# Performance work log

Measured on AMD Instinct MI355X. Metric: run time of the kernel, lower is better.

Reference implementation:

```python
import jax, jax.numpy as jnp
import numpy as np

N_NODES = 50000
N_EDGES = 600000
D_IN = 128
D_OUT = 128
N_BASES = 4
N_RATINGS = 5


def setup_inputs() -> dict:
    key = jax.random.key(0)
    k1, k2, k3, k4, k5, k6 = jax.random.split(key, 6)
    x = jax.random.normal(k1, (N_NODES, D_IN), dtype=jnp.float32)
    edge_index = jax.random.randint(k2, (2, N_EDGES), 0, N_NODES, dtype=jnp.int64)
    edge_type = jax.random.randint(k3, (N_EDGES,), 0, N_RATINGS, dtype=jnp.int64)
    # basis matrices B_k: (out, in); a_r stacked over ratings: (R, K); W_0: (out, in)
    B = jax.random.normal(k4, (N_BASES, D_OUT, D_IN), dtype=jnp.float32) * 0.05
    A = jax.random.normal(k5, (N_RATINGS, N_BASES), dtype=jnp.float32) * 0.05
    W0 = jax.random.normal(k6, (D_OUT, D_IN), dtype=jnp.float32) * 0.05
    return {"x": x, "edge_index": edge_index, "edge_type": edge_type, "B": B, "A": A, "W0": W0}


def reference(x, edge_index, edge_type, B, A, W0):
    # self-loop term: (W0 @ x^T)^T == x @ W0^T
    n_nodes = x.shape[0]
    src, tgt = edge_index[0], edge_index[1]
    out = x @ W0.T  # [N, out]
    # per-relation basis-composed weights W_r = sum_k a_r[k] * B_k  -> [R, out, in]
    W = jnp.einsum('rk,kod->rod', A, B)
    n_ratings = A.shape[0]
    for r in range(n_ratings):  # small fixed relation set
        h = x @ W[r].T                     # [N, out] transform once per node
        msg = jnp.where((edge_type == r)[:, None], h[src], jnp.float32(0))  # [E, out]
        out = out + jax.ops.segment_sum(msg, tgt, num_segments=n_nodes)
    return out
```

## Files before the change

### kernel.cpp

```cpp
#include <hip/hip_runtime.h>

#define N_NODES 50000
#define N_EDGES 600000
#define D 128
#define KTOT 768
#define NB_SCAN 196

typedef __attribute__((ext_vector_type(8))) short short8;
typedef __attribute__((ext_vector_type(4))) float float4v;

static __device__ __forceinline__ float bf2f(unsigned int u16) {
    union { unsigned int i; float f; } v; v.i = u16 << 16; return v.f;
}
static __device__ __forceinline__ unsigned short f2bf(float f) {
    union { float f; unsigned int i; } v; v.f = f;
    unsigned int u = v.i;
    return (unsigned short)((u + 0x7FFFu + ((u >> 16) & 1u)) >> 16);
}
static __device__ __forceinline__ float h2f(unsigned int h) {
    unsigned int s = (h >> 15) & 1u, e = (h >> 10) & 0x1fu, m = h & 0x3ffu;
    unsigned int bits = (e == 0) ? (s << 31)
                                 : ((s << 31) | ((e + 112u) << 23) | (m << 13));
    union { unsigned int i; float f; } v; v.i = bits; return v.f;
}

__global__ __launch_bounds__(256) void setup(int* __restrict__ flags,
                                             int* __restrict__ cnt,
                                             unsigned int* __restrict__ scanst) {
    int i = blockIdx.x * 256 + threadIdx.x;
    if (i < N_NODES) cnt[i] = 0;
    if (i < 8) flags[i] = 0;
    if (i < 200) scanst[i] = 0;
}

__global__ __launch_bounds__(256) void detect_all(const int* __restrict__ ei,
                                                  const int* __restrict__ et,
                                                  const unsigned int* __restrict__ x,
                                                  const unsigned int* __restrict__ B,
                                                  const unsigned int* __restrict__ A,
                                                  const unsigned int* __restrict__ W0,
                                                  int* __restrict__ flags) {
    __shared__ int sflag;
    if (threadIdx.x == 0) sflag = 0;
    __syncthreads();
    int b = blockIdx.x, acc = 0, fidx;
    if (b < 192) {
        fidx = 0;
        for (int i = b * 256 + threadIdx.x; i < N_EDGES; i += 192 * 256)
            acc |= ei[2 * i + 1];
    } else if (b < 240) {
        fidx = 1;
        for (int i = (b - 192) * 256 + threadIdx.x; i < N_EDGES / 2; i += 48 * 256)
            acc |= et[2 * i + 1];
    } else if (b < 288) {
        fidx = 2;
        for (int i = (b - 240) * 256 + threadIdx.x; i < 600000; i += 48 * 256) {
            unsigned int e = (x[i] >> 7) & 0xffu;
            acc |= (e > 0xA0u || e < 0x50u) ? 1 : 0;
        }
    } else if (b < 300) {
        fidx = 3;
        for (int i = (b - 288) * 256 + threadIdx.x; i < 32768; i += 12 * 256) {
            unsigned int e = (B[i] >> 7) & 0xffu;
            acc |= (e > 0xA0u || e < 0x50u) ? 1 : 0;
        }
    } else if (b == 300) {
        fidx = 4;
        for (int i = threadIdx.x; i < 10; i += 256) {
            unsigned int e = (A[i] >> 7) & 0xffu;
            acc |= (e > 0xA0u || e < 0x50u) ? 1 : 0;
        }
    } else if (b < 307) {
        fidx = 5;
        for (int i = (b - 301) * 256 + threadIdx.x; i < 8192; i += 6 * 256) {
            unsigned int e = (W0[i] >> 7) & 0xffu;
            acc |= (e > 0xA0u || e < 0x50u) ? 1 : 0;
        }
    } else {
        fidx = 6;
        for (int i = (b - 307) * 256 + threadIdx.x; i < 300000; i += 48 * 256) {
            unsigned int el = (x[i] >> 7) & 0xffu, eh = (x[i] >> 23) & 0xffu;
            acc |= (el < 0x58u || eh < 0x58u) ? 1 : 0;
        }
    }
    if (acc) sflag = 1;
    __syncthreads();
    if (threadIdx.x == 0 && sflag) atomicOr(flags + fidx, 1);
}

static __device__ __forceinline__ float loadw(const void* p, int idx, int f32) {
    return f32 ? ((const float*)p)[idx] : bf2f(((const unsigned short*)p)[idx]);
}

__global__ __launch_bounds__(256) void norm_hist_conv(const int* __restrict__ ei,
                                                      const int* __restrict__ et,
                                                      int* __restrict__ idx32,
                                                      int* __restrict__ et32,
                                                      int* __restrict__ cnt,
                                                      const void* __restrict__ A,
                                                      const void* __restrict__ B,
                                                      const void* __restrict__ W0,
                                                      unsigned short* __restrict__ wcatB,
                                                      const void* __restrict__ xraw,
                                                      unsigned short* __restrict__ Xcat,
                                                      const int* __restrict__ flags) {
    int b = blockIdx.x;
    if (b < 4688) {
        int i = b * 256 + threadIdx.x;
        if (i < 2 * N_EDGES) {
            int v = flags[0] ? ei[i] : ei[2 * i];
            idx32[i] = v;
            if (i >= N_EDGES && (unsigned)v < (unsigned)N_NODES)
                atomicAdd(&cnt[v], 1);
        }
    } else if (b < 7032) {
        int i = (b - 4688) * 256 + threadIdx.x;
        if (i < N_EDGES) et32[i] = flags[1] ? et[i] : et[2 * i];
    } else if (b < 7416) {
        int idx = (b - 7032) * 256 + threadIdx.x;
        int fB = flags[3], fA = flags[4], fW = flags[5];
        int o = idx / KTOT, k = idx % KTOT;
        float v;
        if (k < D) {
            v = loadw(W0, o * D + k, fW);
        } else {
            int r = (k - D) >> 7, d = (k - D) & 127;
            v = 0.f;
#pragma unroll
            for (int j = 0; j < 4; ++j)
                v += loadw(A, r * 4 + j, fA) * loadw(B, (j * D + o) * D + d, fB);
        }
        wcatB[idx] = f2bf(v);
    } else {
        int idx = (b - 7416) * 256 + threadIdx.x;
        int n = idx >> 5, cg = idx & 31;
        int f32 = flags[2], f16 = flags[6];
        unsigned short o0, o1, o2, o3;
        if (f32) {
            float4 v = *((const float4*)xraw + idx);
            o0 = f2bf(v.x); o1 = f2bf(v.y); o2 = f2bf(v.z); o3 = f2bf(v.w);
        } else {
            uint2 v = *((const uint2*)xraw + idx);
            if (f16) {
                o0 = f2bf(h2f(v.x & 0xffffu)); o1 = f2bf(h2f(v.x >> 16));
                o2 = f2bf(h2f(v.y & 0xffffu)); o3 = f2bf(h2f(v.y >> 16));
            } else {
                o0 = v.x & 0xffffu; o1 = v.x >> 16; o2 = v.y & 0xffffu; o3 = v.y >> 16;
            }
        }
        unsigned long long pack = (unsigned long long)o0 | ((unsigned long long)o1 << 16) |
                                  ((unsigned long long)o2 << 32) | ((unsigned long long)o3 << 48);
        *(unsigned long long*)(Xcat + (size_t)n * KTOT + cg * 4) = pack;
    }
}

__global__ __launch_bounds__(256) void prep_wt6_direct(const void* __restrict__ A,
                                                       const void* __restrict__ B,
                                                       const void* __restrict__ W0,
                                                       float* __restrict__ wcatT6F,
                                                       const int* __restrict__ flags) {
    int idx = blockIdx.x * 256 + threadIdx.x;
    int fB = flags[3], fA = flags[4], fW = flags[5];
    int slot = idx >> 14, d = (idx >> 7) & 127, o = idx & 127;
    float v;
    if (slot == 0) {
        v = loadw(W0, o * D + d, fW);
    } else {
        int r = slot - 1;
        v = 0.f;
#pragma unroll
        for (int j = 0; j < 4; ++j)
            v += loadw(A, r * 4 + j, fA) * loadw(B, (j * D + o) * D + d, fB);
    }
    wcatT6F[idx] = v;
}

#define SC_AGG (1u << 30)
#define SC_PRE (1u << 31)
__global__ __launch_bounds__(256) void scan_fused(const int* __restrict__ cnt,
                                                  int* __restrict__ offsets,
                                                  int* __restrict__ cursor,
                                                  unsigned int* __restrict__ scanst) {
    __shared__ int sh[256];
    __shared__ int sbid, sprefix;
    unsigned int* status = scanst;
    unsigned int* ticket = scanst + 196;
    int t = threadIdx.x;
    if (t == 0) sbid = (int)atomicAdd(ticket, 1u);
    __syncthreads();
    int bid = sbid;
    int idx = bid * 256 + t;
    int v = (idx < N_NODES) ? cnt[idx] : 0;
    sh[t] = v;
    __syncthreads();
    for (int off = 1; off < 256; off <<= 1) {
        int a = (t >= off) ? sh[t - off] : 0;
        __syncthreads();
        sh[t] += a;
        __syncthreads();
    }
    if (t == 0) {
        int total = sh[255];
        atomicExch(&status[bid], (unsigned int)total | SC_AGG);
        int prefix = 0;
        for (int j = bid - 1; j >= 0; --j) {
            unsigned int s;
            do { s = atomicAdd(&status[j], 0u); } while ((s & (SC_AGG | SC_PRE)) == 0u);
            prefix += (int)(s & 0x3FFFFFFFu);
            if (s & SC_PRE) break;
        }
        atomicExch(&status[bid], (unsigned int)(prefix + total) | SC_PRE);
        sprefix = prefix;
    }
    __syncthreads();
    int excl = sh[t] - v + sprefix;
    if (idx < N_NODES) {
        offsets[idx] = excl;
        cursor[idx] = excl;
        if (idx == N_NODES - 1) offsets[N_NODES] = excl + v;
    }
}

__global__ __launch_bounds__(256) void place(const int* __restrict__ src,
                                             const int* __restrict__ tgt,
                                             const int* __restrict__ et,
                                             int* __restrict__ cursor,
                                             int* __restrict__ entries) {
    int e = blockIdx.x * 256 + threadIdx.x;
    if (e >= N_EDGES) return;
    int s = src[e], g = tgt[e], r = et[e];
    if ((unsigned)s >= (unsigned)N_NODES || (unsigned)g >= (unsigned)N_NODES || (unsigned)r >= 5u) return;
    int pos = atomicAdd(&cursor[g], 1);
    entries[pos] = s * 8 + r;
}

#define AGG_ACC2(ent, xw)                                            \
    {                                                                \
        int r_ = (ent) & 7;                                          \
        float flo_ = __uint_as_float((xw) << 16);                    \
        float fhi_ = __uint_as_float((xw) & 0xffff0000u);            \
        if (r_ == 0)      { a0 += flo_; a1 += fhi_; }                \
        else if (r_ == 1) { b0 += flo_; b1 += fhi_; }                \
        else if (r_ == 2) { c0 += flo_; c1 += fhi_; }                \
        else if (r_ == 3) { d0 += flo_; d1 += fhi_; }                \
        else              { e0 += flo_; e1 += fhi_; }                \
    }

static __device__ __forceinline__ unsigned int agg_row_load(
        const unsigned int* __restrict__ Xcat32, int ent, int lane) {
    unsigned int row = (unsigned int)(ent >> 3);
    if (row >= (unsigned)N_NODES) row = 0u;
    return Xcat32[(size_t)row * 384 + lane];
}

__global__ __launch_bounds__(256) void aggregate(const int* __restrict__ offsets,
                                                 const int* __restrict__ entries,
                                                 unsigned int* __restrict__ Xcat32) {
    int tid = threadIdx.x;
    int wid = tid >> 6, lane = tid & 63;
    int n = __builtin_amdgcn_readfirstlane(blockIdx.x * 4 + wid);
    int beg = __builtin_amdgcn_readfirstlane(offsets[n]);
    int end = __builtin_amdgcn_readfirstlane(offsets[n + 1]);
    float a0 = 0, a1 = 0, b0 = 0, b1 = 0, c0 = 0, c1 = 0, d0 = 0, d1 = 0, e0 = 0, e1 = 0;

    for (int base = beg; base < end; base += 64) {
        int cnt = end - base;
        if (cnt > 64) cnt = 64;
        int eload = entries[base + lane];
        int j = 0;
        for (; j + 3 < cnt; j += 4) {
            int en0 = __builtin_amdgcn_readlane(eload, j);
            int en1 = __builtin_amdgcn_readlane(eload, j + 1);
            int en2 = __builtin_amdgcn_readlane(eload, j + 2);
            int en3 = __builtin_amdgcn_readlane(eload, j + 3);
            unsigned int x0 = agg_row_load(Xcat32, en0, lane);
            unsigned int x1 = agg_row_load(Xcat32, en1, lane);
            unsigned int x2 = agg_row_load(Xcat32, en2, lane);
            unsigned int x3 = agg_row_load(Xcat32, en3, lane);
            AGG_ACC2(en0, x0);
            AGG_ACC2(en1, x1);
            AGG_ACC2(en2, x2);
            AGG_ACC2(en3, x3);
        }
        for (; j < cnt; ++j) {
            int en = __builtin_amdgcn_readlane(eload, j);
            unsigned int xw = agg_row_load(Xcat32, en, lane);
            AGG_ACC2(en, xw);
        }
    }

    size_t o = (size_t)n * 384 + 64 + lane;
    Xcat32[o]       = (unsigned int)f2bf(a0) | ((unsigned int)f2bf(a1) << 16);
    Xcat32[o + 64]  = (unsigned int)f2bf(b0) | ((unsigned int)f2bf(b1) << 16);
    Xcat32[o + 128] = (unsigned int)f2bf(c0) | ((unsigned int)f2bf(c1) << 16);
    Xcat32[o + 192] = (unsigned int)f2bf(d0) | ((unsigned int)f2bf(d1) << 16);
    Xcat32[o + 256] = (unsigned int)f2bf(e0) | ((unsigned int)f2bf(e1) << 16);
}

__global__ __launch_bounds__(256) void gemm_mfma(const unsigned short* __restrict__ Xcat,
                                                 const unsigned short* __restrict__ wcatB,
                                                 float* __restrict__ outF) {
    __shared__ unsigned short xs[128 * 72];
    __shared__ unsigned short wsd[128 * 72];
    int tid = threadIdx.x;
    int m0 = blockIdx.x * 128;
    int wid = tid >> 6, lane = tid & 63;
    int wm = (wid & 1) * 64, wn = (wid >> 1) * 64;
    int lm = lane & 15, kg = lane >> 4;
    int srow = tid >> 3, scol = (tid & 7) * 8;

    float4v accf[4][4];
#pragma unroll
    for (int i = 0; i < 4; ++i)
#pragma unroll
        for (int j = 0; j < 4; ++j) accf[i][j] = (float4v){0.f, 0.f, 0.f, 0.f};

    short8 xr[4], wr[4];
    const short8 z8 = {0, 0, 0, 0, 0, 0, 0, 0};
#pragma unroll
    for (int i = 0; i < 4; ++i) {
        int row = srow + i * 32;
        int gm = m0 + row;
        xr[i] = (gm < N_NODES) ? *(const short8*)(Xcat + (size_t)gm * KTOT + scol) : z8;
        wr[i] = *(const short8*)(wcatB + (size_t)row * KTOT + scol);
    }

    for (int kc = 0; kc < 12; ++kc) {
        if (kc) __syncthreads();
#pragma unroll
        for (int i = 0; i < 4; ++i) {
            int row = srow + i * 32;
            *(short8*)(&xs[row * 72 + scol]) = xr[i];
            *(short8*)(&wsd[row * 72 + scol]) = wr[i];
        }
        __syncthreads();
        if (kc + 1 < 12) {
            int kb = (kc + 1) * 64 + scol;
#pragma unroll
            for (int i = 0; i < 4; ++i) {
                int row = srow + i * 32;
                int gm = m0 + row;
                xr[i] = (gm < N_NODES) ? *(const short8*)(Xcat + (size_t)gm * KTOT + kb) : z8;
                wr[i] = *(const short8*)(wcatB + (size_t)row * KTOT + kb);
            }
        }
#pragma unroll
        for (int kb = 0; kb < 2; ++kb) {
            int k = kb * 32 + kg * 8;
            short8 a[4], b[4];
#pragma unroll
            for (int i = 0; i < 4; ++i)
                a[i] = *(const short8*)(&xs[(wm + i * 16 + lm) * 72 + k]);
#pragma unroll
            for (int j = 0; j < 4; ++j)
                b[j] = *(const short8*)(&wsd[(wn + j * 16 + lm) * 72 + k]);
#pragma unroll
            for (int i = 0; i < 4; ++i)
#pragma unroll
                for (int j = 0; j < 4; ++j)
                    accf[i][j] = __builtin_amdgcn_mfma_f32_16x16x32_bf16(a[i], b[j], accf[i][j], 0, 0, 0);
        }
    }

#pragma unroll
    for (int i = 0; i < 4; ++i) {
        int gmb = m0 + wm + i * 16 + kg * 4;
#pragma unroll
        for (int j = 0; j < 4; ++j) {
            int gn = wn + j * 16 + lm;
#pragma unroll
            for (int r = 0; r < 4; ++r) {
                int gm = gmb + r;
                if (gm < N_NODES) outF[(size_t)gm * D + gn] = accf[i][j][r];
            }
        }
    }
}

static __device__ __forceinline__ float2 readx2(const void* x, int node, int lane,
                                                int f32, int f16) {
    if (f32) return *((const float2*)x + (size_t)node * 64 + lane);
    unsigned int w = *((const unsigned int*)x + (size_t)node * 64 + lane);
    float2 r;
    if (f16) { r.x = h2f(w & 0xffffu); r.y = h2f(w >> 16); }
    else     { r.x = bf2f(w & 0xffffu); r.y = bf2f(w >> 16); }
    return r;
}

__global__ __launch_bounds__(256) void self_raw(const void* __restrict__ x,
                                                const float* __restrict__ wcatT6F,
                                                float* __restrict__ outF,
                                                const int* __restrict__ flags) {
    int t = blockIdx.x * 256 + threadIdx.x;
    int n = t >> 6, lane = t & 63;
    int f32 = flags[2], f16 = flags[6];
    float2 xp = readx2(x, n, lane, f32, f16);
    float m0 = 0.f, m1 = 0.f;
#pragma unroll 8
    for (int dp = 0; dp < 64; ++dp) {
        float xa = __shfl(xp.x, dp);
        float xc = __shfl(xp.y, dp);
        float2 w0 = *(const float2*)(wcatT6F + (size_t)(2 * dp) * D + 2 * lane);
        float2 w1 = *(const float2*)(wcatT6F + (size_t)(2 * dp + 1) * D + 2 * lane);
        m0 += xa * w0.x + xc * w1.x;
        m1 += xa * w0.y + xc * w1.y;
    }
    *((float2*)outF + (size_t)n * 64 + lane) = make_float2(m0, m1);
}

__global__ __launch_bounds__(256) void edge_raw(const int* __restrict__ src,
                                                const int* __restrict__ tgt,
                                                const int* __restrict__ et,
                                                const void* __restrict__ x,
                                                const float* __restrict__ wcatT6F,
                                                float* __restrict__ outF,
                                                const int* __restrict__ flags) {
    int t = blockIdx.x * 256 + threadIdx.x;
    int e = t >> 6, lane = t & 63;
    if (e >= N_EDGES) return;
    int f32 = flags[2], f16 = flags[6];
    int s = src[e], g = tgt[e], r = et[e];
    if ((unsigned)s >= (unsigned)N_NODES || (unsigned)g >= (unsigned)N_NODES || (unsigned)r >= 5u) return;
    float2 xp = readx2(x, s, lane, f32, f16);
    const float* wt = wcatT6F + (size_t)(1 + r) * D * D;
    float m0 = 0.f, m1 = 0.f;
#pragma unroll 8
    for (int dp = 0; dp < 64; ++dp) {
        float xa = __shfl(xp.x, dp);
        float xc = __shfl(xp.y, dp);
        float2 w0 = *(const float2*)(wt + (size_t)(2 * dp) * D + 2 * lane);
        float2 w1 = *(const float2*)(wt + (size_t)(2 * dp + 1) * D + 2 * lane);
        m0 += xa * w0.x + xc * w1.x;
        m1 += xa * w0.y + xc * w1.y;
    }
    float* ap = outF + (size_t)g * D + lane * 2;
    atomicAdd(ap + 0, m0);
    atomicAdd(ap + 1, m1);
}

extern "C" void kernel_launch(void* const* d_in, const int* in_sizes, int n_in,
                              void* d_out, int out_size, void* d_ws, size_t ws_size,
                              hipStream_t stream) {
    const void* x  = nullptr; const int* ei = nullptr; const int* et = nullptr;
    const void* B  = nullptr; const void* A = nullptr; const void* W0 = nullptr;
    for (int i = 0; i < n_in; ++i) {
        switch (in_sizes[i]) {
            case 6400000: x  = d_in[i]; break;
            case 1200000: ei = (const int*)d_in[i]; break;
            case 600000:  et = (const int*)d_in[i]; break;
            case 65536:   B  = d_in[i]; break;
            case 20:      A  = d_in[i]; break;
            case 16384:   W0 = d_in[i]; break;
            default: break;
        }
    }
    if (!x || !ei || !et || !B || !A || !W0) {
        x  = d_in[0]; ei = (const int*)d_in[1]; et = (const int*)d_in[2];
        B  = d_in[3]; A  = d_in[4]; W0 = d_in[5];
    }
    float* outF = (float*)d_out;

    char* ws = (char*)d_ws;
    int*   flags   = (int*)(ws + 0);
    float* wcatT6F = (float*)(ws + 256);
    unsigned short* wcatB = (unsigned short*)(ws + 393472);
    int* offsets  = (int*)(ws + 590080);
    int* cursor   = (int*)(ws + 790144);
    int* cnt      = (int*)(ws + 990144);
    unsigned int* scanst = (unsigned int*)(ws + 1190144);
    int* entries  = (int*)(ws + 1191168);
    int* idx32    = (int*)(ws + 3591168);
    int* et32     = (int*)(ws + 8391168);
    unsigned short* Xcat = (unsigned short*)(ws + 10791168);
    const size_t needMain = 10791168ull + 76800000ull;
    const size_t needT3   = 393472ull;

    int* src32 = idx32;
    int* tgt32 = idx32 + N_EDGES;

    setup<<<NB_SCAN, 256, 0, stream>>>(flags, cnt, scanst);
    detect_all<<<355, 256, 0, stream>>>(ei, et, (const unsigned int*)x,
                                        (const unsigned int*)B, (const unsigned int*)A,
                                        (const unsigned int*)W0, flags);

    if (ws_size >= needMain) {
        norm_hist_conv<<<13666, 256, 0, stream>>>(ei, et, idx32, et32, cnt,
                                                  A, B, W0, wcatB, x, Xcat, flags);
        scan_fused<<<NB_SCAN, 256, 0, stream>>>(cnt, offsets, cursor, scanst);
        place<<<2344, 256, 0, stream>>>(src32, tgt32, et32, cursor, entries);
        aggregate<<<12500, 256, 0, stream>>>(offsets, entries, (unsigned int*)Xcat);
        gemm_mfma<<<391, 256, 0, stream>>>(Xcat, wcatB, outF);
    } else if (ws_size >= needT3) {
        prep_wt6_direct<<<384, 256, 0, stream>>>(A, B, W0, wcatT6F, flags);
        self_raw<<<12500, 256, 0, stream>>>(x, wcatT6F, outF, flags);
        edge_raw<<<150000, 256, 0, stream>>>(ei, ei + N_EDGES, et, x, wcatT6F, outF, flags);
    }
}
```

Baseline: 228.5 us.

## Transform nodes first, then gather per-relation transformed rows into output

Reorders the computation from aggregate-then-GEMM to GEMM-then-aggregate. A new MFMA GEMM computes Y = x·[W0;W1..W5]^T per node in bf16 (768 columns). The aggregation then gathers the relation-specific slice of Y for each incoming edge and adds the self term, writing fp32 output directly. This removes the separate x→Xcat conversion and the final 768-K GEMM. The scan and place kernels are merged into one using a grid-wide spin barrier, which depends on all 196 blocks being resident at once. Results are now rounded to bf16 per transformed message before summation, which changes numerics.

```diff
diff --git a/kernel.cpp b/kernel.cpp
--- a/kernel.cpp
+++ b/kernel.cpp
@@ -3,7 +3,6 @@
 #define N_NODES 50000
 #define N_EDGES 600000
 #define D 128
-#define KTOT 768
 #define NB_SCAN 196
 
 typedef __attribute__((ext_vector_type(8))) short short8;
@@ -92,18 +91,16 @@
     return f32 ? ((const float*)p)[idx] : bf2f(((const unsigned short*)p)[idx]);
 }
 
-__global__ __launch_bounds__(256) void norm_hist_conv(const int* __restrict__ ei,
-                                                      const int* __restrict__ et,
-                                                      int* __restrict__ idx32,
-                                                      int* __restrict__ et32,
-                                                      int* __restrict__ cnt,
-                                                      const void* __restrict__ A,
-                                                      const void* __restrict__ B,
-                                                      const void* __restrict__ W0,
-                                                      unsigned short* __restrict__ wcatB,
-                                                      const void* __restrict__ xraw,
-                                                      unsigned short* __restrict__ Xcat,
-                                                      const int* __restrict__ flags) {
+__global__ __launch_bounds__(256) void norm_hist_w(const int* __restrict__ ei,
+                                                   const int* __restrict__ et,
+                                                   int* __restrict__ idx32,
+                                                   int* __restrict__ et32,
+                                                   int* __restrict__ cnt,
+                                                   const void* __restrict__ A,
+                                                   const void* __restrict__ B,
+                                                   const void* __restrict__ W0,
+                                                   unsigned short* __restrict__ wcatW,
+                                                   const int* __restrict__ flags) {
     int b = blockIdx.x;
     if (b < 4688) {
         int i = b * 256 + threadIdx.x;
@@ -116,41 +113,22 @@
     } else if (b < 7032) {
         int i = (b - 4688) * 256 + threadIdx.x;
         if (i < N_EDGES) et32[i] = flags[1] ? et[i] : et[2 * i];
-    } else if (b < 7416) {
+    } else {
         int idx = (b - 7032) * 256 + threadIdx.x;
         int fB = flags[3], fA = flags[4], fW = flags[5];
-        int o = idx / KTOT, k = idx % KTOT;
+        int f = idx >> 7, d = idx & 127;
+        int slot = f >> 7, o = f & 127;
         float v;
-        if (k < D) {
-            v = loadw(W0, o * D + k, fW);
+        if (slot == 0) {
+            v = loadw(W0, o * D + d, fW);
         } else {
-            int r = (k - D) >> 7, d = (k - D) & 127;
+            int r = slot - 1;
             v = 0.f;
 #pragma unroll
             for (int j = 0; j < 4; ++j)
                 v += loadw(A, r * 4 + j, fA) * loadw(B, (j * D + o) * D + d, fB);
         }
-        wcatB[idx] = f2bf(v);
-    } else {
-        int idx = (b - 7416) * 256 + threadIdx.x;
-        int n = idx >> 5, cg = idx & 31;
-        int f32 = flags[2], f16 = flags[6];
-        unsigned short o0, o1, o2, o3;
-        if (f32) {
-            float4 v = *((const float4*)xraw + idx);
-            o0 = f2bf(v.x); o1 = f2bf(v.y); o2 = f2bf(v.z); o3 = f2bf(v.w);
-        } else {
-            uint2 v = *((const uint2*)xraw + idx);
-            if (f16) {
-                o0 = f2bf(h2f(v.x & 0xffffu)); o1 = f2bf(h2f(v.x >> 16));
-                o2 = f2bf(h2f(v.y & 0xffffu)); o3 = f2bf(h2f(v.y >> 16));
-            } else {
-                o0 = v.x & 0xffffu; o1 = v.x >> 16; o2 = v.y & 0xffffu; o3 = v.y >> 16;
-            }
-        }
-        unsigned long long pack = (unsigned long long)o0 | ((unsigned long long)o1 << 16) |
-                                  ((unsigned long long)o2 << 32) | ((unsigned long long)o3 << 48);
-        *(unsigned long long*)(Xcat + (size_t)n * KTOT + cg * 4) = pack;
+        wcatW[idx] = f2bf(v);
     }
 }
 
@@ -175,16 +153,131 @@
     wcatT6F[idx] = v;
 }
 
+__global__ __launch_bounds__(256) void gemm_y(const void* __restrict__ xraw,
+                                              const unsigned short* __restrict__ wcatW,
+                                              unsigned short* __restrict__ Ybf,
+                                              const int* __restrict__ flags) {
+    __shared__ unsigned short xs[64 * 136];
+    __shared__ unsigned short wsd[128 * 136];
+    int tid = threadIdx.x;
+    int m0 = blockIdx.x * 64;
+    int wid = tid >> 6, lane = tid & 63;
+    int wm = (wid & 1) * 32, wn = (wid >> 1) * 64;
+    int lm = lane & 15, kg = lane >> 4;
+    int f32 = flags[2], f16 = flags[6];
+    const short8 z8 = {0, 0, 0, 0, 0, 0, 0, 0};
+
+    {
+        int row = tid >> 2, cseg = (tid & 3) * 32;
+        int gm = m0 + row;
+        short8 av[4];
+        if (gm >= N_NODES) {
+#pragma unroll
+            for (int q = 0; q < 4; ++q) av[q] = z8;
+        } else if (f32) {
+            const float4* xp = (const float4*)xraw + (((size_t)gm * D + cseg) >> 2);
+#pragma unroll
+            for (int q = 0; q < 4; ++q) {
+                float4 u0 = xp[2 * q], u1 = xp[2 * q + 1];
+                union { short8 s; unsigned short h[8]; } pk;
+                pk.h[0] = f2bf(u0.x); pk.h[1] = f2bf(u0.y);
+                pk.h[2] = f2bf(u0.z); pk.h[3] = f2bf(u0.w);
+                pk.h[4] = f2bf(u1.x); pk.h[5] = f2bf(u1.y);
+                pk.h[6] = f2bf(u1.z); pk.h[7] = f2bf(u1.w);
+                av[q] = pk.s;
+            }
+        } else if (f16) {
+            const uint4* xp4 = (const uint4*)xraw + (((size_t)gm * D + cseg) >> 3);
+#pragma unroll
+            for (int q = 0; q < 4; ++q) {
+                uint4 u = xp4[q];
+                unsigned int ww[4] = {u.x, u.y, u.z, u.w};
+                union { short8 s; unsigned short h[8]; } pk;
+#pragma unroll
+                for (int z = 0; z < 4; ++z) {
+                    pk.h[2 * z]     = f2bf(h2f(ww[z] & 0xffffu));
+                    pk.h[2 * z + 1] = f2bf(h2f(ww[z] >> 16));
+                }
+                av[q] = pk.s;
+            }
+        } else {
+            const uint4* xp4 = (const uint4*)xraw + (((size_t)gm * D + cseg) >> 3);
+#pragma unroll
+            for (int q = 0; q < 4; ++q) {
+                union { uint4 v; short8 s; } cv; cv.v = xp4[q];
+                av[q] = cv.s;
+            }
+        }
+#pragma unroll
+        for (int q = 0; q < 4; ++q)
+            *(short8*)(&xs[row * 136 + cseg + q * 8]) = av[q];
+    }
+
+    for (int nt = 0; nt < 6; ++nt) {
+        if (nt) __syncthreads();
+        {
+            int row = tid >> 1, cseg = (tid & 1) * 64;
+            const unsigned short* wp = wcatW + (size_t)(nt * 128 + row) * D + cseg;
+#pragma unroll
+            for (int q = 0; q < 8; ++q)
+                *(short8*)(&wsd[row * 136 + cseg + q * 8]) = *(const short8*)(wp + q * 8);
+        }
+        __syncthreads();
+
+        float4v accf[2][4];
+#pragma unroll
+        for (int i = 0; i < 2; ++i)
+#pragma unroll
+            for (int j = 0; j < 4; ++j) accf[i][j] = (float4v){0.f, 0.f, 0.f, 0.f};
+
+#pragma unroll
+        for (int kb = 0; kb < 4; ++kb) {
+            int k = kb * 32 + kg * 8;
+            short8 a[2], b[4];
+#pragma unroll
+            for (int i = 0; i < 2; ++i)
+                a[i] = *(const short8*)(&xs[(wm + i * 16 + lm) * 136 + k]);
+#pragma unroll
+            for (int j = 0; j < 4; ++j)
+                b[j] = *(const short8*)(&wsd[(wn + j * 16 + lm) * 136 + k]);
+#pragma unroll
+            for (int i = 0; i < 2; ++i)
+#pragma unroll
+                for (int j = 0; j < 4; ++j)
+                    accf[i][j] = __builtin_amdgcn_mfma_f32_16x16x32_bf16(a[i], b[j], accf[i][j], 0, 0, 0);
+        }
+
+#pragma unroll
+        for (int i = 0; i < 2; ++i) {
+            int gmb = m0 + wm + i * 16 + kg * 4;
+#pragma unroll
+            for (int j = 0; j < 4; ++j) {
+                int gn = nt * 128 + wn + j * 16 + lm;
+#pragma unroll
+                for (int r = 0; r < 4; ++r) {
+                    int gm = gmb + r;
+                    if (gm < N_NODES) Ybf[(size_t)gm * 768 + gn] = f2bf(accf[i][j][r]);
+                }
+            }
+        }
+    }
+}
+
 #define SC_AGG (1u << 30)
 #define SC_PRE (1u << 31)
-__global__ __launch_bounds__(256) void scan_fused(const int* __restrict__ cnt,
+__global__ __launch_bounds__(256) void scan_place(const int* __restrict__ cnt,
                                                   int* __restrict__ offsets,
                                                   int* __restrict__ cursor,
-                                                  unsigned int* __restrict__ scanst) {
+                                                  unsigned int* __restrict__ scanst,
+                                                  const int* __restrict__ src,
+                                                  const int* __restrict__ tgt,
+                                                  const int* __restrict__ et,
+                                                  int* __restrict__ entries) {
     __shared__ int sh[256];
     __shared__ int sbid, sprefix;
     unsigned int* status = scanst;
     unsigned int* ticket = scanst + 196;
+    unsigned int* done   = scanst + 197;
     int t = threadIdx.x;
     if (t == 0) sbid = (int)atomicAdd(ticket, 1u);
     __syncthreads();
@@ -216,52 +309,36 @@
     int excl = sh[t] - v + sprefix;
     if (idx < N_NODES) {
         offsets[idx] = excl;
-        cursor[idx] = excl;
+        atomicExch(&cursor[idx], excl);
         if (idx == N_NODES - 1) offsets[N_NODES] = excl + v;
     }
-}
-
-__global__ __launch_bounds__(256) void place(const int* __restrict__ src,
-                                             const int* __restrict__ tgt,
-                                             const int* __restrict__ et,
-                                             int* __restrict__ cursor,
-                                             int* __restrict__ entries) {
-    int e = blockIdx.x * 256 + threadIdx.x;
-    if (e >= N_EDGES) return;
-    int s = src[e], g = tgt[e], r = et[e];
-    if ((unsigned)s >= (unsigned)N_NODES || (unsigned)g >= (unsigned)N_NODES || (unsigned)r >= 5u) return;
-    int pos = atomicAdd(&cursor[g], 1);
-    entries[pos] = s * 8 + r;
-}
-
-#define AGG_ACC2(ent, xw)                                            \
-    {                                                                \
-        int r_ = (ent) & 7;                                          \
-        float flo_ = __uint_as_float((xw) << 16);                    \
-        float fhi_ = __uint_as_float((xw) & 0xffff0000u);            \
-        if (r_ == 0)      { a0 += flo_; a1 += fhi_; }                \
-        else if (r_ == 1) { b0 += flo_; b1 += fhi_; }                \
-        else if (r_ == 2) { c0 += flo_; c1 += fhi_; }                \
-        else if (r_ == 3) { d0 += flo_; d1 += fhi_; }                \
-        else              { e0 += flo_; e1 += fhi_; }                \
-    }
-
-static __device__ __forceinline__ unsigned int agg_row_load(
-        const unsigned int* __restrict__ Xcat32, int ent, int lane) {
-    unsigned int row = (unsigned int)(ent >> 3);
-    if (row >= (unsigned)N_NODES) row = 0u;
-    return Xcat32[(size_t)row * 384 + lane];
-}
-
-__global__ __launch_bounds__(256) void aggregate(const int* __restrict__ offsets,
-                                                 const int* __restrict__ entries,
-                                                 unsigned int* __restrict__ Xcat32) {
+    __syncthreads();
+    if (t == 0) {
+        atomicAdd(done, 1u);
+        while (atomicAdd(done, 0u) < (unsigned)NB_SCAN) __builtin_amdgcn_s_sleep(1);
+    }
+    __syncthreads();
+    int e0 = bid * 3062;
+    int e1 = e0 + 3062; if (e1 > N_EDGES) e1 = N_EDGES;
+    for (int e = e0 + t; e < e1; e += 256) {
+        int s = src[e], g = tgt[e], r = et[e];
+        if ((unsigned)s >= (unsigned)N_NODES || (unsigned)g >= (unsigned)N_NODES || (unsigned)r >= 5u) continue;
+        int pos = atomicAdd(&cursor[g], 1);
+        entries[pos] = s * 8 + r;
+    }
+}
+
+__global__ __launch_bounds__(256) void agg_out(const int* __restrict__ offsets,
+                                               const int* __restrict__ entries,
+                                               const unsigned int* __restrict__ Y32,
+                                               float* __restrict__ outF) {
     int tid = threadIdx.x;
     int wid = tid >> 6, lane = tid & 63;
     int n = __builtin_amdgcn_readfirstlane(blockIdx.x * 4 + wid);
     int beg = __builtin_amdgcn_readfirstlane(offsets[n]);
     int end = __builtin_amdgcn_readfirstlane(offsets[n + 1]);
-    float a0 = 0, a1 = 0, b0 = 0, b1 = 0, c0 = 0, c1 = 0, d0 = 0, d1 = 0, e0 = 0, e1 = 0;
+    unsigned int selfw = Y32[(size_t)n * 384 + lane];
+    float a0 = bf2f(selfw & 0xffffu), a1 = bf2f(selfw >> 16);
 
     for (int base = beg; base < end; base += 64) {
         int cnt = end - base;
@@ -273,108 +350,28 @@
             int en1 = __builtin_amdgcn_readlane(eload, j + 1);
             int en2 = __builtin_amdgcn_readlane(eload, j + 2);
             int en3 = __builtin_amdgcn_readlane(eload, j + 3);
-            unsigned int x0 = agg_row_load(Xcat32, en0, lane);
-            unsigned int x1 = agg_row_load(Xcat32, en1, lane);
-            unsigned int x2 = agg_row_load(Xcat32, en2, lane);
-            unsigned int x3 = agg_row_load(Xcat32, en3, lane);
-            AGG_ACC2(en0, x0);
-            AGG_ACC2(en1, x1);
-            AGG_ACC2(en2, x2);
-            AGG_ACC2(en3, x3);
+            unsigned int r0 = (unsigned)(en0 >> 3) < (unsigned)N_NODES ? (unsigned)(en0 >> 3) : 0u;
+            unsigned int r1 = (unsigned)(en1 >> 3) < (unsigned)N_NODES ? (unsigned)(en1 >> 3) : 0u;
+            unsigned int r2 = (unsigned)(en2 >> 3) < (unsigned)N_NODES ? (unsigned)(en2 >> 3) : 0u;
+            unsigned int r3 = (unsigned)(en3 >> 3) < (unsigned)N_NODES ? (unsigned)(en3 >> 3) : 0u;
+            unsigned int x0 = Y32[(size_t)r0 * 384 + ((en0 & 7) + 1) * 64 + lane];
+            unsigned int x1 = Y32[(size_t)r1 * 384 + ((en1 & 7) + 1) * 64 + lane];
+            unsigned int x2 = Y32[(size_t)r2 * 384 + ((en2 & 7) + 1) * 64 + lane];
+            unsigned int x3 = Y32[(size_t)r3 * 384 + ((en3 & 7) + 1) * 64 + lane];
+            a0 += bf2f(x0 & 0xffffu); a1 += bf2f(x0 >> 16);
+            a0 += bf2f(x1 & 0xffffu); a1 += bf2f(x1 >> 16);
+            a0 += bf2f(x2 & 0xffffu); a1 += bf2f(x2 >> 16);
+            a0 += bf2f(x3 & 0xffffu); a1 += bf2f(x3 >> 16);
         }
         for (; j < cnt; ++j) {
             int en = __builtin_amdgcn_readlane(eload, j);
-            unsigned int xw = agg_row_load(Xcat32, en, lane);
-            AGG_ACC2(en, xw);
-        }
-    }
-
-    size_t o = (size_t)n * 384 + 64 + lane;
-    Xcat32[o]       = (unsigned int)f2bf(a0) | ((unsigned int)f2bf(a1) << 16);
-    Xcat32[o + 64]  = (unsigned int)f2bf(b0) | ((unsigned int)f2bf(b1) << 16);
-    Xcat32[o + 128] = (unsigned int)f2bf(c0) | ((unsigned int)f2bf(c1) << 16);
-    Xcat32[o + 192] = (unsigned int)f2bf(d0) | ((unsigned int)f2bf(d1) << 16);
-    Xcat32[o + 256] = (unsigned int)f2bf(e0) | ((unsigned int)f2bf(e1) << 16);
-}
-
-__global__ __launch_bounds__(256) void gemm_mfma(const unsigned short* __restrict__ Xcat,
-                                                 const unsigned short* __restrict__ wcatB,
-                                                 float* __restrict__ outF) {
-    __shared__ unsigned short xs[128 * 72];
-    __shared__ unsigned short wsd[128 * 72];
-    int tid = threadIdx.x;
-    int m0 = blockIdx.x * 128;
-    int wid = tid >> 6, lane = tid & 63;
-    int wm = (wid & 1) * 64, wn = (wid >> 1) * 64;
-    int lm = lane & 15, kg = lane >> 4;
-    int srow = tid >> 3, scol = (tid & 7) * 8;
-
-    float4v accf[4][4];
-#pragma unroll
-    for (int i = 0; i < 4; ++i)
-#pragma unroll
-        for (int j = 0; j < 4; ++j) accf[i][j] = (float4v){0.f, 0.f, 0.f, 0.f};
-
-    short8 xr[4], wr[4];
-    const short8 z8 = {0, 0, 0, 0, 0, 0, 0, 0};
-#pragma unroll
-    for (int i = 0; i < 4; ++i) {
-        int row = srow + i * 32;
-        int gm = m0 + row;
-        xr[i] = (gm < N_NODES) ? *(const short8*)(Xcat + (size_t)gm * KTOT + scol) : z8;
-        wr[i] = *(const short8*)(wcatB + (size_t)row * KTOT + scol);
-    }
-
-    for (int kc = 0; kc < 12; ++kc) {
-        if (kc) __syncthreads();
-#pragma unroll
-        for (int i = 0; i < 4; ++i) {
-            int row = srow + i * 32;
-            *(short8*)(&xs[row * 72 + scol]) = xr[i];
-            *(short8*)(&wsd[row * 72 + scol]) = wr[i];
-        }
-        __syncthreads();
-        if (kc + 1 < 12) {
-            int kb = (kc + 1) * 64 + scol;
-#pragma unroll
-            for (int i = 0; i < 4; ++i) {
-                int row = srow + i * 32;
-                int gm = m0 + row;
-                xr[i] = (gm < N_NODES) ? *(const short8*)(Xcat + (size_t)gm * KTOT + kb) : z8;
-                wr[i] = *(const short8*)(wcatB + (size_t)row * KTOT + kb);
-            }
-        }
-#pragma unroll
-        for (int kb = 0; kb < 2; ++kb) {
-            int k = kb * 32 + kg * 8;
-            short8 a[4], b[4];
-#pragma unroll
-            for (int i = 0; i < 4; ++i)
-                a[i] = *(const short8*)(&xs[(wm + i * 16 + lm) * 72 + k]);
-#pragma unroll
-            for (int j = 0; j < 4; ++j)
-                b[j] = *(const short8*)(&wsd[(wn + j * 16 + lm) * 72 + k]);
-#pragma unroll
-            for (int i = 0; i < 4; ++i)
-#pragma unroll
-                for (int j = 0; j < 4; ++j)
-                    accf[i][j] = __builtin_amdgcn_mfma_f32_16x16x32_bf16(a[i], b[j], accf[i][j], 0, 0, 0);
-        }
-    }
-
-#pragma unroll
-    for (int i = 0; i < 4; ++i) {
-        int gmb = m0 + wm + i * 16 + kg * 4;
-#pragma unroll
-        for (int j = 0; j < 4; ++j) {
-            int gn = wn + j * 16 + lm;
-#pragma unroll
-            for (int r = 0; r < 4; ++r) {
-                int gm = gmb + r;
-                if (gm < N_NODES) outF[(size_t)gm * D + gn] = accf[i][j][r];
-            }
-        }
-    }
+            unsigned int rr = (unsigned)(en >> 3) < (unsigned)N_NODES ? (unsigned)(en >> 3) : 0u;
+            unsigned int xw = Y32[(size_t)rr * 384 + ((en & 7) + 1) * 64 + lane];
+            a0 += bf2f(xw & 0xffffu); a1 += bf2f(xw >> 16);
+        }
+    }
+
+    *((float2*)outF + (size_t)n * 64 + lane) = make_float2(a0, a1);
 }
 
 static __device__ __forceinline__ float2 readx2(const void* x, int node, int lane,
@@ -463,7 +460,7 @@
     char* ws = (char*)d_ws;
     int*   flags   = (int*)(ws + 0);
     float* wcatT6F = (float*)(ws + 256);
-    unsigned short* wcatB = (unsigned short*)(ws + 393472);
+    unsigned short* wcatW = (unsigned short*)(ws + 393472);
     int* offsets  = (int*)(ws + 590080);
     int* cursor   = (int*)(ws + 790144);
     int* cnt      = (int*)(ws + 990144);
@@ -471,7 +468,7 @@
     int* entries  = (int*)(ws + 1191168);
     int* idx32    = (int*)(ws + 3591168);
     int* et32     = (int*)(ws + 8391168);
-    unsigned short* Xcat = (unsigned short*)(ws + 10791168);
+    unsigned short* Y = (unsigned short*)(ws + 10791168);
     const size_t needMain = 10791168ull + 76800000ull;
     const size_t needT3   = 393472ull;
 
@@ -484,12 +481,12 @@
                                         (const unsigned int*)W0, flags);
 
     if (ws_size >= needMain) {
-        norm_hist_conv<<<13666, 256, 0, stream>>>(ei, et, idx32, et32, cnt,
-                                                  A, B, W0, wcatB, x, Xcat, flags);
-        scan_fused<<<NB_SCAN, 256, 0, stream>>>(cnt, offsets, cursor, scanst);
-        place<<<2344, 256, 0, stream>>>(src32, tgt32, et32, cursor, entries);
-        aggregate<<<12500, 256, 0, stream>>>(offsets, entries, (unsigned int*)Xcat);
-        gemm_mfma<<<391, 256, 0, stream>>>(Xcat, wcatB, outF);
+        norm_hist_w<<<7416, 256, 0, stream>>>(ei, et, idx32, et32, cnt,
+                                              A, B, W0, wcatW, flags);
+        gemm_y<<<782, 256, 0, stream>>>(x, wcatW, Y, flags);
+        scan_place<<<NB_SCAN, 256, 0, stream>>>(cnt, offsets, cursor, scanst,
+                                                src32, tgt32, et32, entries);
+        agg_out<<<12500, 256, 0, stream>>>(offsets, entries, (const unsigned int*)Y, outF);
     } else if (ws_size >= needT3) {
         prep_wt6_direct<<<384, 256, 0, stream>>>(A, B, W0, wcatT6F, flags);
         self_raw<<<12500, 256, 0, stream>>>(x, wcatT6F, outF, flags);
```

New measurement: 242.0 us. +5.9%, slower.

## Use direct global-to-LDS loads with XOR swizzle and 64-row tiles in GEMM

Applied to the files above, without the earlier changes.

Rewrites the final MFMA GEMM to stage tiles with global_load_lds (direct global-to-LDS copies) instead of register staging. The LDS layout becomes an XOR-swizzled 128-byte row, replacing the old padding, to avoid bank conflicts. The M tile is halved to 64 rows, doubling the grid to 782 blocks for better CU occupancy. The register prefetch of the next K chunk is dropped, so each iteration waits on vmcnt(0) with no overlap between loads and MFMA. The bounds check on rows is removed, so the workspace requirement grows to allow reads past the last node.

```diff
diff --git a/kernel.cpp b/kernel.cpp
--- a/kernel.cpp
+++ b/kernel.cpp
@@ -297,65 +297,66 @@
     Xcat32[o + 256] = (unsigned int)f2bf(e0) | ((unsigned int)f2bf(e1) << 16);
 }
 
+static __device__ __forceinline__ void gload16(const void* g, void* l) {
+    __builtin_amdgcn_global_load_lds(
+        (const __attribute__((address_space(1))) unsigned int*)g,
+        (__attribute__((address_space(3))) unsigned int*)l, 16, 0, 0);
+}
+
 __global__ __launch_bounds__(256) void gemm_mfma(const unsigned short* __restrict__ Xcat,
                                                  const unsigned short* __restrict__ wcatB,
                                                  float* __restrict__ outF) {
-    __shared__ unsigned short xs[128 * 72];
-    __shared__ unsigned short wsd[128 * 72];
+    __shared__ __align__(16) unsigned short xs[64 * 64];
+    __shared__ __align__(16) unsigned short wsd[128 * 64];
     int tid = threadIdx.x;
-    int m0 = blockIdx.x * 128;
+    int m0 = blockIdx.x * 64;
     int wid = tid >> 6, lane = tid & 63;
-    int wm = (wid & 1) * 64, wn = (wid >> 1) * 64;
+    int wm = (wid & 1) * 32, wn = (wid >> 1) * 64;
     int lm = lane & 15, kg = lane >> 4;
-    int srow = tid >> 3, scol = (tid & 7) * 8;
-
-    float4v accf[4][4];
-#pragma unroll
-    for (int i = 0; i < 4; ++i)
+
+    int srow = lane >> 3;
+    int schunk = (lane & 7) ^ srow;
+    const char* xgb = (const char*)Xcat + (size_t)(m0 + wid * 8 + srow) * (KTOT * 2) + schunk * 16;
+    const char* wgb = (const char*)wcatB + (size_t)(wid * 8 + srow) * (KTOT * 2) + schunk * 16;
+    char* xlb = (char*)xs + (wid * 8) * 128;
+    char* wlb = (char*)wsd + (wid * 8) * 128;
+
+    float4v accf[2][4];
+#pragma unroll
+    for (int i = 0; i < 2; ++i)
 #pragma unroll
         for (int j = 0; j < 4; ++j) accf[i][j] = (float4v){0.f, 0.f, 0.f, 0.f};
-
-    short8 xr[4], wr[4];
-    const short8 z8 = {0, 0, 0, 0, 0, 0, 0, 0};
-#pragma unroll
-    for (int i = 0; i < 4; ++i) {
-        int row = srow + i * 32;
-        int gm = m0 + row;
-        xr[i] = (gm < N_NODES) ? *(const short8*)(Xcat + (size_t)gm * KTOT + scol) : z8;
-        wr[i] = *(const short8*)(wcatB + (size_t)row * KTOT + scol);
-    }
 
     for (int kc = 0; kc < 12; ++kc) {
         if (kc) __syncthreads();
-#pragma unroll
-        for (int i = 0; i < 4; ++i) {
-            int row = srow + i * 32;
-            *(short8*)(&xs[row * 72 + scol]) = xr[i];
-            *(short8*)(&wsd[row * 72 + scol]) = wr[i];
-        }
+        {
+            size_t ko = (size_t)kc * 128;
+            gload16(xgb + ko, xlb);
+            gload16(xgb + ko + 32 * (KTOT * 2), xlb + 32 * 128);
+            gload16(wgb + ko, wlb);
+            gload16(wgb + ko + 32 * (KTOT * 2), wlb + 32 * 128);
+            gload16(wgb + ko + 64 * (KTOT * 2), wlb + 64 * 128);
+            gload16(wgb + ko + 96 * (KTOT * 2), wlb + 96 * 128);
+        }
+        asm volatile("s_waitcnt vmcnt(0)" ::: "memory");
         __syncthreads();
-        if (kc + 1 < 12) {
-            int kb = (kc + 1) * 64 + scol;
-#pragma unroll
-            for (int i = 0; i < 4; ++i) {
-                int row = srow + i * 32;
-                int gm = m0 + row;
-                xr[i] = (gm < N_NODES) ? *(const short8*)(Xcat + (size_t)gm * KTOT + kb) : z8;
-                wr[i] = *(const short8*)(wcatB + (size_t)row * KTOT + kb);
+
+#pragma unroll
+        for (int kb = 0; kb < 2; ++kb) {
+            int kchunk = kb * 4 + kg;
+            short8 a[2], b[4];
+#pragma unroll
+            for (int i = 0; i < 2; ++i) {
+                int ra = wm + i * 16 + lm;
+                a[i] = *(const short8*)((const char*)xs + ra * 128 + ((kchunk ^ (ra & 7)) * 16));
             }
-        }
-#pragma unroll
-        for (int kb = 0; kb < 2; ++kb) {
-            int k = kb * 32 + kg * 8;
-            short8 a[4], b[4];
-#pragma unroll
-            for (int i = 0; i < 4; ++i)
-                a[i] = *(const short8*)(&xs[(wm + i * 16 + lm) * 72 + k]);
-#pragma unroll
-            for (int j = 0; j < 4; ++j)
-                b[j] = *(const short8*)(&wsd[(wn + j * 16 + lm) * 72 + k]);
-#pragma unroll
-            for (int i = 0; i < 4; ++i)
+#pragma unroll
+            for (int j = 0; j < 4; ++j) {
+                int rb = wn + j * 16 + lm;
+                b[j] = *(const short8*)((const char*)wsd + rb * 128 + ((kchunk ^ (rb & 7)) * 16));
+            }
+#pragma unroll
+            for (int i = 0; i < 2; ++i)
 #pragma unroll
                 for (int j = 0; j < 4; ++j)
                     accf[i][j] = __builtin_amdgcn_mfma_f32_16x16x32_bf16(a[i], b[j], accf[i][j], 0, 0, 0);
@@ -363,7 +364,7 @@
     }
 
 #pragma unroll
-    for (int i = 0; i < 4; ++i) {
+    for (int i = 0; i < 2; ++i) {
         int gmb = m0 + wm + i * 16 + kg * 4;
 #pragma unroll
         for (int j = 0; j < 4; ++j) {
@@ -472,7 +473,7 @@
     int* idx32    = (int*)(ws + 3591168);
     int* et32     = (int*)(ws + 8391168);
     unsigned short* Xcat = (unsigned short*)(ws + 10791168);
-    const size_t needMain = 10791168ull + 76800000ull;
+    const size_t needMain = 10791168ull + 76800000ull + 131072ull;
     const size_t needT3   = 393472ull;
 
     int* src32 = idx32;
@@ -489,7 +490,7 @@
         scan_fused<<<NB_SCAN, 256, 0, stream>>>(cnt, offsets, cursor, scanst);
         place<<<2344, 256, 0, stream>>>(src32, tgt32, et32, cursor, entries);
         aggregate<<<12500, 256, 0, stream>>>(offsets, entries, (unsigned int*)Xcat);
-        gemm_mfma<<<391, 256, 0, stream>>>(Xcat, wcatB, outF);
+        gemm_mfma<<<782, 256, 0, stream>>>(Xcat, wcatB, outF);
     } else if (ws_size >= needT3) {
         prep_wt6_direct<<<384, 256, 0, stream>>>(A, B, W0, wcatT6F, flags);
         self_raw<<<12500, 256, 0, stream>>>(x, wcatT6F, outF, flags);
```

Result: slower. 233.2 us (+2.0%).
